# Performance work log

Measured on AMD Instinct MI355X. Metric: run time of the kernel, lower is better.

Reference implementation:

```python
import jax, jax.numpy as jnp
import numpy as np

N = 100000
E = 1600000
D_IN = 128
D_OUT = 128

def setup_inputs() -> dict:
    key = jax.random.key(0)
    k1, k2, k3, k4, k5, k6 = jax.random.split(key, 6)
    h = jax.random.normal(k1, (N, D_IN), dtype=jnp.float32)
    # norm ~ deg^{-1/2}; use positive uniform values as stand-in
    norm = jax.random.uniform(k2, (N, 1), dtype=jnp.float32, minval=0.05, maxval=1.0)
    src = jax.random.randint(k3, (E,), 0, N, dtype=jnp.int32)
    dst = jax.random.randint(k4, (E,), 0, N, dtype=jnp.int32)
    weight = jax.random.normal(k5, (D_IN, D_OUT), dtype=jnp.float32) * (2.0 / (D_IN + D_OUT)) ** 0.5
    bias = jnp.zeros((D_OUT,), dtype=jnp.float32)
    return {"h": h, "norm": norm, "src": src, "dst": dst, "weight": weight, "bias": bias}

def reference(h, norm, src, dst, weight, bias):
    n_nodes = h.shape[0]
    hw = h @ weight                      # [N, D_out] dense GEMM
    hw = hw * norm                       # pre-aggregation degree scale
    msgs = hw[src]                       # gather: [E, D_out]
    agg = jax.ops.segment_sum(msgs, dst, num_segments=n_nodes)  # scatter-sum
    out = agg * norm + bias              # post-scale + bias
    return out
```

## Files before the change

kernel.cpp:

```cpp
#include <hip/hip_runtime.h>
#include <hip/hip_bf16.h>

#define D 128
#define D4 32
#define CHUNK 3072
#define MAXB 2048
#define NSEG 8

typedef __attribute__((ext_vector_type(8))) short bf16x8;
typedef __attribute__((ext_vector_type(4))) float f32x4;

static __device__ __forceinline__ unsigned short f2bf(float f) {
    unsigned u = __float_as_uint(f);
    u += 0x7FFFu + ((u >> 16) & 1u);
    return (unsigned short)(u >> 16);
}
static __device__ __forceinline__ float bf2f(unsigned short u) {
    return __uint_as_float(((unsigned)u) << 16);
}

__global__ __launch_bounds__(256) void gemm_mfma_kernel(
    const float* __restrict__ h, const float* __restrict__ W,
    const float* __restrict__ norm, unsigned short* __restrict__ hwb,
    int n_nodes)
{
    __shared__ unsigned short As[64 * 136];
    __shared__ unsigned short Bs[128 * 136];

    const int t = threadIdx.x;
    const int row0 = blockIdx.x * 64;

    #pragma unroll
    for (int i = 0; i < 16; ++i) {
        const int idx = t + 256 * i;
        const int k = idx >> 5;
        const int c = (idx & 31) * 4;
        const float4 w = ((const float4*)W)[idx];
        Bs[(c + 0) * 136 + k] = f2bf(w.x);
        Bs[(c + 1) * 136 + k] = f2bf(w.y);
        Bs[(c + 2) * 136 + k] = f2bf(w.z);
        Bs[(c + 3) * 136 + k] = f2bf(w.w);
    }
    #pragma unroll
    for (int i = 0; i < 8; ++i) {
        const int idx = t + 256 * i;
        const int r = idx >> 5;
        const int kq = idx & 31;
        long gr = row0 + r; if (gr >= n_nodes) gr = n_nodes - 1;
        const float4 a = ((const float4*)(h + gr * D))[kq];
        ushort4 o;
        o.x = f2bf(a.x); o.y = f2bf(a.y); o.z = f2bf(a.z); o.w = f2bf(a.w);
        *(ushort4*)&As[r * 136 + kq * 4] = o;
    }
    __syncthreads();

    const int wv = t >> 6;
    const int lane = t & 63;
    const int m = lane & 15;
    const int quad = lane >> 4;

    f32x4 acc[8];
    #pragma unroll
    for (int nt = 0; nt < 8; ++nt) { f32x4 z = {0.f, 0.f, 0.f, 0.f}; acc[nt] = z; }

    #pragma unroll
    for (int kt = 0; kt < 4; ++kt) {
        const bf16x8 af = *(const bf16x8*)&As[(wv * 16 + m) * 136 + kt * 32 + quad * 8];
        #pragma unroll
        for (int nt = 0; nt < 8; ++nt) {
            const bf16x8 bfr = *(const bf16x8*)&Bs[(nt * 16 + m) * 136 + kt * 32 + quad * 8];
            acc[nt] = __builtin_amdgcn_mfma_f32_16x16x32_bf16(af, bfr, acc[nt], 0, 0, 0);
        }
    }

    float nv[4];
    #pragma unroll
    for (int i = 0; i < 4; ++i) {
        const int gr = row0 + wv * 16 + quad * 4 + i;
        nv[i] = (gr < n_nodes) ? norm[gr] : 0.f;
    }
    #pragma unroll
    for (int nt = 0; nt < 8; ++nt) {
        #pragma unroll
        for (int i = 0; i < 4; ++i) {
            const int gr = row0 + wv * 16 + quad * 4 + i;
            if (gr < n_nodes)
                hwb[(size_t)gr * D + nt * 16 + m] = f2bf(acc[nt][i] * nv[i]);
        }
    }
}

__global__ __launch_bounds__(1024) void hist_kernel(
    const int* __restrict__ dst, int* __restrict__ H,
    unsigned short* __restrict__ hwb, int n_edges, int n_nodes)
{
    __shared__ int lbh[MAXB];
    const int t = threadIdx.x;
    const int g = blockIdx.x;
    for (int i = t; i < MAXB; i += 1024) lbh[i] = 0;
    if (g == 0 && t < 32) {
        ushort4 z; z.x = z.y = z.z = z.w = 0;
        ((ushort4*)(hwb + (size_t)n_nodes * D))[t] = z;
    }
    __syncthreads();
    const int e0 = g * CHUNK;
    const int e1 = min(e0 + CHUNK, n_edges);
    for (int e = e0 + t; e < e1; e += 1024) {
        atomicAdd(&lbh[dst[e] >> 6], 1);
    }
    __syncthreads();
    for (int i = t; i < MAXB; i += 1024) {
        H[(size_t)g * MAXB + i] = lbh[i];
    }
}

__global__ __launch_bounds__(256) void colsum_kernel(
    const int* __restrict__ H, int* __restrict__ PS, int eb)
{
    const int col = blockIdx.x * 256 + threadIdx.x;
    const int seg = blockIdx.y;
    const int glen = (eb + NSEG - 1) / NSEG;
    const int g0 = seg * glen;
    const int g1 = min(g0 + glen, eb);
    int s = 0;
    for (int g = g0; g < g1; ++g) s += H[(size_t)g * MAXB + col];
    PS[seg * MAXB + col] = s;
}

__global__ __launch_bounds__(256) void bucket_scan_kernel(
    const int* __restrict__ PS, int* __restrict__ boff, int* __restrict__ bcur)
{
    __shared__ int tmp[256];
    const int t = threadIdx.x;
    int v[8];
    int s = 0;
    #pragma unroll
    for (int k = 0; k < 8; ++k) {
        const int i = t * 8 + k;
        int c = 0;
        #pragma unroll
        for (int sg = 0; sg < NSEG; ++sg) c += PS[sg * MAXB + i];
        v[k] = c; s += c;
    }
    tmp[t] = s;
    __syncthreads();
    for (int ofs = 1; ofs < 256; ofs <<= 1) {
        int x = (t >= ofs) ? tmp[t - ofs] : 0;
        __syncthreads();
        tmp[t] += x;
        __syncthreads();
    }
    int run = tmp[t] - s;
    #pragma unroll
    for (int k = 0; k < 8; ++k) {
        boff[t * 8 + k] = run;
        bcur[t * 8 + k] = run;
        run += v[k];
    }
    if (t == 255) boff[MAXB] = run;
}

__global__ __launch_bounds__(1024) void bscatter_kernel(
    const int* __restrict__ src, const int* __restrict__ dst,
    const int* __restrict__ H, int* __restrict__ bcur,
    unsigned int* __restrict__ ebuf, int n_edges)
{
    __shared__ int lbh[MAXB];
    __shared__ int lofs[MAXB];
    const int t = threadIdx.x;
    const int g = blockIdx.x;
    for (int i = t; i < MAXB; i += 1024) {
        lbh[i] = 0;
        const int c = H[(size_t)g * MAXB + i];
        lofs[i] = c ? atomicAdd(&bcur[i], c) : 0;
    }
    __syncthreads();
    const int e0 = g * CHUNK;
    const int e1 = min(e0 + CHUNK, n_edges);
    for (int e = e0 + t; e < e1; e += 1024) {
        const int d = dst[e];
        const int bk = d >> 6;
        const int r = atomicAdd(&lbh[bk], 1);
        ebuf[lofs[bk] + r] = (unsigned)src[e] | ((unsigned)(d & 63) << 17);
    }
}

__global__ __launch_bounds__(256) void fill_local_kernel(
    const unsigned int* __restrict__ ebuf, const int* __restrict__ boff,
    int* __restrict__ off, int* __restrict__ cnt,
    int* __restrict__ srcs, int n_nodes)
{
    __shared__ int lcnt[64];
    __shared__ int lcur[64];
    __shared__ int loff[64];
    const int t = threadIdx.x;
    const int b = blockIdx.x;
    const int gn0 = b * 64;
    if (t < 64) lcnt[t] = 0;
    __syncthreads();
    const int e0 = boff[b], e1 = boff[b + 1];
    for (int e = e0 + t; e < e1; e += 256) {
        atomicAdd(&lcnt[(ebuf[e] >> 17) & 63], 1);
    }
    __syncthreads();
    if (t < 64) {
        const int c = lcnt[t];
        const int p = (c + 7) & ~7;
        int x = p;
        #pragma unroll
        for (int ofs = 1; ofs < 64; ofs <<= 1) {
            const int y = __shfl_up(x, ofs, 64);
            if (t >= ofs) x += y;
        }
        const int base = boff[b] + b * 448 + (x - p);
        lcur[t] = base;
        loff[t] = base;
        const int gn = gn0 + t;
        if (gn < n_nodes) { cnt[gn] = c; off[gn] = base; }
    }
    __syncthreads();
    for (int e = e0 + t; e < e1; e += 256) {
        const unsigned rec = ebuf[e];
        const int loc = (rec >> 17) & 63;
        const int pos = atomicAdd(&lcur[loc], 1);
        srcs[pos] = (int)(rec & 0x1FFFFu);
    }
    for (int w = t; w < 512; w += 256) {
        const int ln = w >> 3, k = w & 7;
        const int gn = gn0 + ln;
        if (gn < n_nodes) {
            const int c = lcnt[ln];
            const int pad = (8 - (c & 7)) & 7;
            if (k < pad) srcs[loff[ln] + c + k] = n_nodes;
        }
    }
}

__global__ __launch_bounds__(256) void agg_kernel(
    const unsigned short* __restrict__ hwb, const int* __restrict__ srcs,
    const int* __restrict__ off, const int* __restrict__ cnt,
    const float* __restrict__ norm, const float* __restrict__ bias,
    float* __restrict__ out, int n_nodes)
{
    const int t = threadIdx.x;
    const int sub = t >> 5;
    const int lane32 = t & 31;
    const int node = blockIdx.x * 8 + sub;
    if (node >= n_nodes) return;

    const int start = off[node];
    const int deg = cnt[node];
    const int nb8 = (deg + 7) >> 3;

    const ushort4* hw4 = (const ushort4*)hwb;

    float4 acc; acc.x = acc.y = acc.z = acc.w = 0.0f;
    int myidx = 0;

    for (int b = 0; b < nb8; ++b) {
        const int q = b & 3;
        if (q == 0) myidx = srcs[start + b * 8 + lane32];
        ushort4 v[8];
        #pragma unroll
        for (int jj = 0; jj < 8; ++jj) {
            const int s = __shfl(myidx, q * 8 + jj, 32);
            v[jj] = hw4[(long)s * D4 + lane32];
        }
        #pragma unroll
        for (int jj = 0; jj < 8; ++jj) {
            acc.x += bf2f(v[jj].x);
            acc.y += bf2f(v[jj].y);
            acc.z += bf2f(v[jj].z);
            acc.w += bf2f(v[jj].w);
        }
    }

    const float nv = norm[node];
    const float4 bs = ((const float4*)bias)[lane32];
    float4 o;
    o.x = acc.x * nv + bs.x;
    o.y = acc.y * nv + bs.y;
    o.z = acc.z * nv + bs.z;
    o.w = acc.w * nv + bs.w;
    ((float4*)out)[(long)node * D4 + lane32] = o;
}

__global__ __launch_bounds__(256) void scatter_kernel(
    const unsigned short* __restrict__ hwb, const int* __restrict__ src,
    const int* __restrict__ dst, float* __restrict__ out, int n_edges)
{
    const int idx = blockIdx.x * 256 + threadIdx.x;
    if (idx >= n_edges * D4) return;
    const int e = idx >> 5;
    const int g = idx & 31;
    const int s = src[e];
    const int d = dst[e];
    const ushort4 v = ((const ushort4*)hwb)[(long)s * D4 + g];
    float* o = out + (long)d * D + g * 4;
    atomicAdd(o + 0, bf2f(v.x));
    atomicAdd(o + 1, bf2f(v.y));
    atomicAdd(o + 2, bf2f(v.z));
    atomicAdd(o + 3, bf2f(v.w));
}

__global__ __launch_bounds__(256) void finalize_kernel(
    float* __restrict__ out, const float* __restrict__ norm,
    const float* __restrict__ bias, int n_nodes)
{
    const int idx = blockIdx.x * 256 + threadIdx.x;
    if (idx >= n_nodes * D4) return;
    const int n = idx >> 5;
    const int g = idx & 31;
    float4 v = ((float4*)out)[idx];
    const float nv = norm[n];
    const float4 b = ((const float4*)bias)[g];
    v.x = v.x * nv + b.x;
    v.y = v.y * nv + b.y;
    v.z = v.z * nv + b.z;
    v.w = v.w * nv + b.w;
    ((float4*)out)[idx] = v;
}

extern "C" void kernel_launch(void* const* d_in, const int* in_sizes, int n_in,
                              void* d_out, int out_size, void* d_ws, size_t ws_size,
                              hipStream_t stream) {
    const float* h    = (const float*)d_in[0];
    const float* norm = (const float*)d_in[1];
    const int*   src  = (const int*)d_in[2];
    const int*   dst  = (const int*)d_in[3];
    const float* W    = (const float*)d_in[4];
    const float* bias = (const float*)d_in[5];
    float* out = (float*)d_out;

    const int n_nodes = in_sizes[1];
    const int n_edges = in_sizes[2];

    const int NBUCK = (n_nodes + 63) >> 6;
    const int EB    = (n_edges + CHUNK - 1) / CHUNK;
    const int srcs_len = n_edges + 448 * NBUCK + 64;

    size_t p = 0;
    auto take = [&](size_t bytes) {
        size_t cur = p;
        p += (bytes + 255) & ~(size_t)255;
        return cur;
    };
    const size_t hwb_off  = take(((size_t)n_nodes + 1) * D * sizeof(unsigned short));
    const size_t cnt_off  = take((size_t)n_nodes * sizeof(int));
    const size_t off_off  = take((size_t)n_nodes * sizeof(int));
    const size_t srcs_off = take((size_t)srcs_len * sizeof(int));
    const size_t ebuf_off = take((size_t)n_edges * sizeof(unsigned int));
    const size_t boff_off = take((MAXB + 1) * sizeof(int));
    const size_t bcur_off = take(MAXB * sizeof(int));
    const size_t H_off    = take((size_t)EB * MAXB * sizeof(int));
    const size_t PS_off   = take((size_t)NSEG * MAXB * sizeof(int));
    const size_t needed = p;

    char* ws = (char*)d_ws;
    unsigned short* hwb = (unsigned short*)(ws + hwb_off);

    gemm_mfma_kernel<<<(n_nodes + 63) / 64, 256, 0, stream>>>(h, W, norm, hwb, n_nodes);

    if (ws_size >= needed && NBUCK <= MAXB && n_nodes <= 131072) {
        int* cnt   = (int*)(ws + cnt_off);
        int* off   = (int*)(ws + off_off);
        int* srcs  = (int*)(ws + srcs_off);
        unsigned int* ebuf = (unsigned int*)(ws + ebuf_off);
        int* boff  = (int*)(ws + boff_off);
        int* bcur  = (int*)(ws + bcur_off);
        int* H     = (int*)(ws + H_off);
        int* PS    = (int*)(ws + PS_off);

        hist_kernel<<<EB, 1024, 0, stream>>>(dst, H, hwb, n_edges, n_nodes);
        colsum_kernel<<<dim3(MAXB / 256, NSEG), 256, 0, stream>>>(H, PS, EB);
        bucket_scan_kernel<<<1, 256, 0, stream>>>(PS, boff, bcur);
        bscatter_kernel<<<EB, 1024, 0, stream>>>(src, dst, H, bcur, ebuf, n_edges);
        fill_local_kernel<<<NBUCK, 256, 0, stream>>>(ebuf, boff, off, cnt, srcs, n_nodes);
        agg_kernel<<<(n_nodes + 7) / 8, 256, 0, stream>>>(hwb, srcs, off, cnt, norm, bias,
                                                          out, n_nodes);
    } else {
        hipMemsetAsync(d_out, 0, (size_t)out_size * sizeof(float), stream);
        const int work = n_edges * D4;
        scatter_kernel<<<(work + 255) / 256, 256, 0, stream>>>(hwb, src, dst, out, n_edges);
        const int work2 = n_nodes * D4;
        finalize_kernel<<<(work2 + 255) / 256, 256, 0, stream>>>(out, norm, bias, n_nodes);
    }
}
```

Baseline: 265.3 us.

## Fuse bucket sort and aggregation into one cooperative persistent kernel

Replaces the chain of six launches (histogram, column sums, scan, scatter, local fill, aggregate) with one cooperative kernel that uses grid-wide syncs between phases. Edge indices are kept in registers between histogram and scatter, and per-bucket source lists are staged in LDS before aggregation. The aim is to remove launch gaps and avoid re-reading src/dst. In exchange each block uses large LDS and 1024 threads, so few blocks fit per CU, and grid.sync has its own cost.

```diff
diff --git a/kernel.cpp b/kernel.cpp
--- a/kernel.cpp
+++ b/kernel.cpp
@@ -1,11 +1,17 @@
 #include <hip/hip_runtime.h>
 #include <hip/hip_bf16.h>
+#include <hip/hip_cooperative_groups.h>
+
+namespace cg = cooperative_groups;
 
 #define D 128
 #define D4 32
 #define CHUNK 3072
+#define CHUNK_C 3200
+#define KSLOT 4
 #define MAXB 2048
 #define NSEG 8
+#define SLDS 8192
 
 typedef __attribute__((ext_vector_type(8))) short bf16x8;
 typedef __attribute__((ext_vector_type(4))) float f32x4;
@@ -86,6 +92,202 @@
             const int gr = row0 + wv * 16 + quad * 4 + i;
             if (gr < n_nodes)
                 hwb[(size_t)gr * D + nt * 16 + m] = f2bf(acc[nt][i] * nv[i]);
+        }
+    }
+}
+
+__global__ __launch_bounds__(1024, 8) void coop_kernel(
+    const int* __restrict__ src, const int* __restrict__ dst,
+    int* __restrict__ H, int* __restrict__ PS, int* __restrict__ SB,
+    int* __restrict__ boff, int* __restrict__ CO,
+    unsigned int* __restrict__ ebuf, int* __restrict__ srcs_g,
+    unsigned short* __restrict__ hwb,
+    const float* __restrict__ norm, const float* __restrict__ bias,
+    float* __restrict__ out,
+    int n_edges, int n_nodes, int EB, int NBUCK)
+{
+    __shared__ int lbh[MAXB];
+    __shared__ int tmp[1024];
+    __shared__ int slds[SLDS];
+    __shared__ int lcnt[64];
+    __shared__ int lcur[64];
+    __shared__ int loffL[64];
+
+    cg::grid_group grid = cg::this_grid();
+    const int t = threadIdx.x;
+    const int g = blockIdx.x;
+    const int gid = g * 1024 + t;
+    const int glen = (EB + NSEG - 1) / NSEG;
+
+    for (int i = t; i < MAXB; i += 1024) lbh[i] = 0;
+    if (g == 0 && t < 32) {
+        ushort4 z; z.x = z.y = z.z = z.w = 0;
+        ((ushort4*)(hwb + (size_t)n_nodes * D))[t] = z;
+    }
+    __syncthreads();
+    const int e0 = g * CHUNK_C;
+    const int e1 = min(e0 + CHUNK_C, n_edges);
+    int ed[KSLOT], es[KSLOT], er[KSLOT];
+    bool ok[KSLOT];
+    #pragma unroll
+    for (int k = 0; k < KSLOT; ++k) {
+        const int e = e0 + t + 1024 * k;
+        ok[k] = e < e1;
+        if (ok[k]) {
+            ed[k] = dst[e];
+            es[k] = src[e];
+            er[k] = atomicAdd(&lbh[ed[k] >> 6], 1);
+        } else { ed[k] = 0; es[k] = 0; er[k] = 0; }
+    }
+    __syncthreads();
+    for (int i = t; i < MAXB; i += 1024) H[(size_t)g * MAXB + i] = lbh[i];
+    grid.sync();
+
+    if (gid < NSEG * MAXB) {
+        const int seg = gid >> 11;
+        const int c = gid & (MAXB - 1);
+        const int g0 = seg * glen, g1 = min(g0 + glen, EB);
+        int s = 0;
+        for (int gg = g0; gg < g1; ++gg) s += H[(size_t)gg * MAXB + c];
+        PS[seg * MAXB + c] = s;
+    }
+    grid.sync();
+
+    if (g == 0) {
+        const int cA = 2 * t, cB = 2 * t + 1;
+        int va = 0, vb = 0;
+        #pragma unroll
+        for (int sg = 0; sg < NSEG; ++sg) { va += PS[sg * MAXB + cA]; vb += PS[sg * MAXB + cB]; }
+        tmp[t] = va + vb;
+        __syncthreads();
+        for (int ofs = 1; ofs < 1024; ofs <<= 1) {
+            const int x = (t >= ofs) ? tmp[t - ofs] : 0;
+            __syncthreads();
+            tmp[t] += x;
+            __syncthreads();
+        }
+        const int run = tmp[t] - (va + vb);
+        boff[cA] = run;
+        boff[cB] = run + va;
+        if (t == 1023) boff[MAXB] = tmp[1023];
+        int sb = run;
+        #pragma unroll
+        for (int sg = 0; sg < NSEG; ++sg) { SB[sg * MAXB + cA] = sb; sb += PS[sg * MAXB + cA]; }
+        sb = run + va;
+        #pragma unroll
+        for (int sg = 0; sg < NSEG; ++sg) { SB[sg * MAXB + cB] = sb; sb += PS[sg * MAXB + cB]; }
+    }
+    grid.sync();
+
+    if (gid < NSEG * MAXB) {
+        const int seg = gid >> 11;
+        const int c = gid & (MAXB - 1);
+        const int g0 = seg * glen, g1 = min(g0 + glen, EB);
+        int run = SB[seg * MAXB + c];
+        for (int gg = g0; gg < g1; ++gg) {
+            CO[(size_t)gg * MAXB + c] = run;
+            run += H[(size_t)gg * MAXB + c];
+        }
+    }
+    grid.sync();
+
+    for (int i = t; i < MAXB; i += 1024) lbh[i] = CO[(size_t)g * MAXB + i];
+    __syncthreads();
+    #pragma unroll
+    for (int k = 0; k < KSLOT; ++k) {
+        if (ok[k])
+            ebuf[lbh[ed[k] >> 6] + er[k]] =
+                (unsigned)es[k] | ((unsigned)(ed[k] & 63) << 17);
+    }
+    grid.sync();
+
+    const ushort4* hw4 = (const ushort4*)hwb;
+    for (int bkt = g; bkt < NBUCK; bkt += gridDim.x) {
+        __syncthreads();
+        if (t < 64) lcnt[t] = 0;
+        __syncthreads();
+        const int w0 = boff[bkt], w1 = boff[bkt + 1];
+        const int wlen = w1 - w0;
+        const bool uselds = (wlen + 480) <= SLDS;
+        const int gbase = w0 + 448 * bkt;
+        for (int e = w0 + t; e < w1; e += 1024)
+            atomicAdd(&lcnt[(ebuf[e] >> 17) & 63], 1);
+        __syncthreads();
+        if (t < 64) {
+            const int c = lcnt[t];
+            const int p = (c + 7) & ~7;
+            int x = p;
+            #pragma unroll
+            for (int ofs = 1; ofs < 64; ofs <<= 1) {
+                const int y = __shfl_up(x, ofs, 64);
+                if (t >= ofs) x += y;
+            }
+            const int base = x - p;
+            lcur[t] = base;
+            loffL[t] = base;
+        }
+        __syncthreads();
+        for (int e = w0 + t; e < w1; e += 1024) {
+            const unsigned rec = ebuf[e];
+            const int loc = (rec >> 17) & 63;
+            const int pos = atomicAdd(&lcur[loc], 1);
+            const int sv = (int)(rec & 0x1FFFFu);
+            if (uselds) slds[pos] = sv; else srcs_g[gbase + pos] = sv;
+        }
+        for (int w = t; w < 512; w += 1024) {
+            const int ln = w >> 3, k = w & 7;
+            const int gn = bkt * 64 + ln;
+            if (gn < n_nodes) {
+                const int c = lcnt[ln];
+                const int pad = (8 - (c & 7)) & 7;
+                if (k < pad) {
+                    const int pos = loffL[ln] + c + k;
+                    if (uselds) slds[pos] = n_nodes; else srcs_g[gbase + pos] = n_nodes;
+                }
+            }
+        }
+        __syncthreads();
+
+        const int grp = t >> 5;
+        const int l = t & 31;
+        #pragma unroll
+        for (int nn = 0; nn < 2; ++nn) {
+            const int loc = grp * 2 + nn;
+            const int gn = bkt * 64 + loc;
+            if (gn >= n_nodes) continue;
+            const int start = loffL[loc];
+            const int deg = lcnt[loc];
+            const int nb8 = (deg + 7) >> 3;
+            float4 acc; acc.x = acc.y = acc.z = acc.w = 0.f;
+            int myidx = 0;
+            for (int b = 0; b < nb8; ++b) {
+                const int q = b & 3;
+                if (q == 0) {
+                    const int ri = start + b * 8 + l;
+                    myidx = uselds ? slds[ri] : srcs_g[gbase + ri];
+                }
+                ushort4 v[8];
+                #pragma unroll
+                for (int jj = 0; jj < 8; ++jj) {
+                    const int s = __shfl(myidx, q * 8 + jj, 32);
+                    v[jj] = hw4[(long)s * D4 + l];
+                }
+                #pragma unroll
+                for (int jj = 0; jj < 8; ++jj) {
+                    acc.x += bf2f(v[jj].x);
+                    acc.y += bf2f(v[jj].y);
+                    acc.z += bf2f(v[jj].z);
+                    acc.w += bf2f(v[jj].w);
+                }
+            }
+            const float nv = norm[gn];
+            const float4 bs = ((const float4*)bias)[l];
+            float4 o;
+            o.x = acc.x * nv + bs.x;
+            o.y = acc.y * nv + bs.y;
+            o.z = acc.z * nv + bs.z;
+            o.w = acc.w * nv + bs.w;
+            ((float4*)out)[(long)gn * D4 + l] = o;
         }
     }
 }
@@ -336,7 +538,9 @@
     const int n_edges = in_sizes[2];
 
     const int NBUCK = (n_nodes + 63) >> 6;
-    const int EB    = (n_edges + CHUNK - 1) / CHUNK;
+    const int EB2   = (n_edges + CHUNK - 1) / CHUNK;
+    const int EBC   = (n_edges + CHUNK_C - 1) / CHUNK_C;
+    const int EBmax = (EB2 > EBC) ? EB2 : EBC;
     const int srcs_len = n_edges + 448 * NBUCK + 64;
 
     size_t p = 0;
@@ -352,8 +556,10 @@
     const size_t ebuf_off = take((size_t)n_edges * sizeof(unsigned int));
     const size_t boff_off = take((MAXB + 1) * sizeof(int));
     const size_t bcur_off = take(MAXB * sizeof(int));
-    const size_t H_off    = take((size_t)EB * MAXB * sizeof(int));
+    const size_t H_off    = take((size_t)EBmax * MAXB * sizeof(int));
     const size_t PS_off   = take((size_t)NSEG * MAXB * sizeof(int));
+    const size_t SB_off   = take((size_t)NSEG * MAXB * sizeof(int));
+    const size_t CO_off   = take((size_t)EBmax * MAXB * sizeof(int));
     const size_t needed = p;
 
     char* ws = (char*)d_ws;
@@ -361,7 +567,46 @@
 
     gemm_mfma_kernel<<<(n_nodes + 63) / 64, 256, 0, stream>>>(h, W, norm, hwb, n_nodes);
 
-    if (ws_size >= needed && NBUCK <= MAXB && n_nodes <= 131072) {
+    static int s_blocks_per_cu = -1;
+    static int s_ncu = 0;
+    if (s_blocks_per_cu < 0) {
+        int nb = 0;
+        if (hipOccupancyMaxActiveBlocksPerMultiprocessor(&nb, coop_kernel, 1024, 0) != hipSuccess)
+            nb = 0;
+        int dev = 0;
+        hipGetDevice(&dev);
+        int ncu = 0;
+        if (hipDeviceGetAttribute(&ncu, hipDeviceAttributeMultiprocessorCount, dev) != hipSuccess)
+            ncu = 0;
+        s_blocks_per_cu = nb;
+        s_ncu = ncu;
+    }
+
+    const bool ws_ok = (ws_size >= needed) && (NBUCK <= MAXB) && (n_nodes <= 131072);
+    const bool coop_ok = ws_ok && EBC >= 16 && EBC <= 512 &&
+                         (long)EBC <= (long)s_blocks_per_cu * (long)s_ncu;
+
+    if (coop_ok) {
+        int* cnt   = (int*)(ws + cnt_off);   (void)cnt;
+        int* off   = (int*)(ws + off_off);   (void)off;
+        int* srcs  = (int*)(ws + srcs_off);
+        unsigned int* ebuf = (unsigned int*)(ws + ebuf_off);
+        int* boff  = (int*)(ws + boff_off);
+        int* H     = (int*)(ws + H_off);
+        int* PS    = (int*)(ws + PS_off);
+        int* SBp   = (int*)(ws + SB_off);
+        int* CO    = (int*)(ws + CO_off);
+
+        int ne = n_edges, nn = n_nodes, eb = EBC, nbk = NBUCK;
+        void* args[] = {
+            (void*)&src, (void*)&dst, (void*)&H, (void*)&PS, (void*)&SBp,
+            (void*)&boff, (void*)&CO, (void*)&ebuf, (void*)&srcs, (void*)&hwb,
+            (void*)&norm, (void*)&bias, (void*)&out,
+            (void*)&ne, (void*)&nn, (void*)&eb, (void*)&nbk
+        };
+        hipLaunchCooperativeKernel((void*)coop_kernel, dim3(EBC), dim3(1024),
+                                   args, 0, stream);
+    } else if (ws_ok && EB2 <= 1024) {
         int* cnt   = (int*)(ws + cnt_off);
         int* off   = (int*)(ws + off_off);
         int* srcs  = (int*)(ws + srcs_off);
@@ -371,10 +616,10 @@
         int* H     = (int*)(ws + H_off);
         int* PS    = (int*)(ws + PS_off);
 
-        hist_kernel<<<EB, 1024, 0, stream>>>(dst, H, hwb, n_edges, n_nodes);
-        colsum_kernel<<<dim3(MAXB / 256, NSEG), 256, 0, stream>>>(H, PS, EB);
+        hist_kernel<<<EB2, 1024, 0, stream>>>(dst, H, hwb, n_edges, n_nodes);
+        colsum_kernel<<<dim3(MAXB / 256, NSEG), 256, 0, stream>>>(H, PS, EB2);
         bucket_scan_kernel<<<1, 256, 0, stream>>>(PS, boff, bcur);
-        bscatter_kernel<<<EB, 1024, 0, stream>>>(src, dst, H, bcur, ebuf, n_edges);
+        bscatter_kernel<<<EB2, 1024, 0, stream>>>(src, dst, H, bcur, ebuf, n_edges);
         fill_local_kernel<<<NBUCK, 256, 0, stream>>>(ebuf, boff, off, cnt, srcs, n_nodes);
         agg_kernel<<<(n_nodes + 7) / 8, 256, 0, stream>>>(hwb, srcs, off, cnt, norm, bias,
                                                           out, n_nodes);
```

After: 263.5 us. No clear change (-0.7%).

## Fuse local CSR fill with aggregation and pre-transpose weight to bf16

Applied to the files above, without the earlier changes.

Merges fill_local and agg kernels so each 64-node bucket builds its source list in LDS and immediately aggregates, removing the global srcs/off/cnt round trip and one launch. The weight fp32-to-bf16 transpose now runs once in a small kernel instead of in every GEMM block, which instead load it with vector copies. In exchange the aggregation runs on only NBUCK (~1563) blocks that each process 64 nodes serially per group, so latency hiding and load balance may be worse. Each block also now uses 16KB more LDS, which can lower occupancy.

```diff
diff --git a/kernel.cpp b/kernel.cpp
--- a/kernel.cpp
+++ b/kernel.cpp
@@ -6,8 +6,10 @@
 #define CHUNK 3072
 #define MAXB 2048
 #define NSEG 8
+#define SL 4096
 
 typedef __attribute__((ext_vector_type(8))) short bf16x8;
+typedef __attribute__((ext_vector_type(8))) unsigned short ushort8;
 typedef __attribute__((ext_vector_type(4))) float f32x4;
 
 static __device__ __forceinline__ unsigned short f2bf(float f) {
@@ -19,8 +21,21 @@
     return __uint_as_float(((unsigned)u) << 16);
 }
 
+__global__ __launch_bounds__(256) void wcvt_kernel(
+    const float* __restrict__ W, unsigned short* __restrict__ Wt)
+{
+    const int idx = blockIdx.x * 256 + threadIdx.x;
+    const float4 w = ((const float4*)W)[idx];
+    const int k = idx >> 5;
+    const int c = (idx & 31) * 4;
+    Wt[(c + 0) * 128 + k] = f2bf(w.x);
+    Wt[(c + 1) * 128 + k] = f2bf(w.y);
+    Wt[(c + 2) * 128 + k] = f2bf(w.z);
+    Wt[(c + 3) * 128 + k] = f2bf(w.w);
+}
+
 __global__ __launch_bounds__(256) void gemm_mfma_kernel(
-    const float* __restrict__ h, const float* __restrict__ W,
+    const float* __restrict__ h, const unsigned short* __restrict__ Wt,
     const float* __restrict__ norm, unsigned short* __restrict__ hwb,
     int n_nodes)
 {
@@ -31,15 +46,12 @@
     const int row0 = blockIdx.x * 64;
 
     #pragma unroll
-    for (int i = 0; i < 16; ++i) {
+    for (int i = 0; i < 8; ++i) {
         const int idx = t + 256 * i;
-        const int k = idx >> 5;
-        const int c = (idx & 31) * 4;
-        const float4 w = ((const float4*)W)[idx];
-        Bs[(c + 0) * 136 + k] = f2bf(w.x);
-        Bs[(c + 1) * 136 + k] = f2bf(w.y);
-        Bs[(c + 2) * 136 + k] = f2bf(w.z);
-        Bs[(c + 3) * 136 + k] = f2bf(w.w);
+        const int c = idx >> 4;
+        const int k8 = idx & 15;
+        const ushort8 w = ((const ushort8*)Wt)[idx];
+        *(ushort8*)&Bs[c * 136 + k8 * 8] = w;
     }
     #pragma unroll
     for (int i = 0; i < 8; ++i) {
@@ -185,21 +197,28 @@
     }
 }
 
-__global__ __launch_bounds__(256) void fill_local_kernel(
+__global__ __launch_bounds__(256) void fillagg_kernel(
     const unsigned int* __restrict__ ebuf, const int* __restrict__ boff,
-    int* __restrict__ off, int* __restrict__ cnt,
-    int* __restrict__ srcs, int n_nodes)
-{
+    int* __restrict__ srcs_g, const unsigned short* __restrict__ hwb,
+    const float* __restrict__ norm, const float* __restrict__ bias,
+    float* __restrict__ out, int n_nodes)
+{
+    __shared__ int slds[SL];
     __shared__ int lcnt[64];
     __shared__ int lcur[64];
     __shared__ int loff[64];
     const int t = threadIdx.x;
     const int b = blockIdx.x;
     const int gn0 = b * 64;
+
     if (t < 64) lcnt[t] = 0;
     __syncthreads();
-    const int e0 = boff[b], e1 = boff[b + 1];
-    for (int e = e0 + t; e < e1; e += 256) {
+    const int w0 = boff[b], w1 = boff[b + 1];
+    const int wlen = w1 - w0;
+    const bool uselds = (wlen + 480) <= SL;
+    const int gbase = w0 + 448 * b;
+
+    for (int e = w0 + t; e < w1; e += 256) {
         atomicAdd(&lcnt[(ebuf[e] >> 17) & 63], 1);
     }
     __syncthreads();
@@ -212,18 +231,17 @@
             const int y = __shfl_up(x, ofs, 64);
             if (t >= ofs) x += y;
         }
-        const int base = boff[b] + b * 448 + (x - p);
+        const int base = x - p;
         lcur[t] = base;
         loff[t] = base;
-        const int gn = gn0 + t;
-        if (gn < n_nodes) { cnt[gn] = c; off[gn] = base; }
-    }
-    __syncthreads();
-    for (int e = e0 + t; e < e1; e += 256) {
+    }
+    __syncthreads();
+    for (int e = w0 + t; e < w1; e += 256) {
         const unsigned rec = ebuf[e];
         const int loc = (rec >> 17) & 63;
         const int pos = atomicAdd(&lcur[loc], 1);
-        srcs[pos] = (int)(rec & 0x1FFFFu);
+        const int sv = (int)(rec & 0x1FFFFu);
+        if (uselds) slds[pos] = sv; else srcs_g[gbase + pos] = sv;
     }
     for (int w = t; w < 512; w += 256) {
         const int ln = w >> 3, k = w & 7;
@@ -231,58 +249,55 @@
         if (gn < n_nodes) {
             const int c = lcnt[ln];
             const int pad = (8 - (c & 7)) & 7;
-            if (k < pad) srcs[loff[ln] + c + k] = n_nodes;
+            if (k < pad) {
+                const int pos = loff[ln] + c + k;
+                if (uselds) slds[pos] = n_nodes; else srcs_g[gbase + pos] = n_nodes;
+            }
         }
     }
-}
-
-__global__ __launch_bounds__(256) void agg_kernel(
-    const unsigned short* __restrict__ hwb, const int* __restrict__ srcs,
-    const int* __restrict__ off, const int* __restrict__ cnt,
-    const float* __restrict__ norm, const float* __restrict__ bias,
-    float* __restrict__ out, int n_nodes)
-{
-    const int t = threadIdx.x;
-    const int sub = t >> 5;
-    const int lane32 = t & 31;
-    const int node = blockIdx.x * 8 + sub;
-    if (node >= n_nodes) return;
-
-    const int start = off[node];
-    const int deg = cnt[node];
-    const int nb8 = (deg + 7) >> 3;
+    __syncthreads();
 
     const ushort4* hw4 = (const ushort4*)hwb;
-
-    float4 acc; acc.x = acc.y = acc.z = acc.w = 0.0f;
-    int myidx = 0;
-
-    for (int b = 0; b < nb8; ++b) {
-        const int q = b & 3;
-        if (q == 0) myidx = srcs[start + b * 8 + lane32];
-        ushort4 v[8];
-        #pragma unroll
-        for (int jj = 0; jj < 8; ++jj) {
-            const int s = __shfl(myidx, q * 8 + jj, 32);
-            v[jj] = hw4[(long)s * D4 + lane32];
+    const int grp = t >> 5;
+    const int l = t & 31;
+    const float4 bs = ((const float4*)bias)[l];
+    for (int nn = 0; nn < 8; ++nn) {
+        const int loc = grp * 8 + nn;
+        const int gn = gn0 + loc;
+        if (gn >= n_nodes) continue;
+        const int start = loff[loc];
+        const int deg = lcnt[loc];
+        const int nb8 = (deg + 7) >> 3;
+        float4 acc; acc.x = acc.y = acc.z = acc.w = 0.f;
+        int myidx = 0;
+        for (int bb = 0; bb < nb8; ++bb) {
+            const int q = bb & 3;
+            if (q == 0) {
+                const int ri = start + bb * 8 + l;
+                myidx = uselds ? slds[ri] : srcs_g[gbase + ri];
+            }
+            ushort4 v[8];
+            #pragma unroll
+            for (int jj = 0; jj < 8; ++jj) {
+                const int s = __shfl(myidx, q * 8 + jj, 32);
+                v[jj] = hw4[(long)s * D4 + l];
+            }
+            #pragma unroll
+            for (int jj = 0; jj < 8; ++jj) {
+                acc.x += bf2f(v[jj].x);
+                acc.y += bf2f(v[jj].y);
+                acc.z += bf2f(v[jj].z);
+                acc.w += bf2f(v[jj].w);
+            }
         }
-        #pragma unroll
-        for (int jj = 0; jj < 8; ++jj) {
-            acc.x += bf2f(v[jj].x);
-            acc.y += bf2f(v[jj].y);
-            acc.z += bf2f(v[jj].z);
-            acc.w += bf2f(v[jj].w);
-        }
-    }
-
-    const float nv = norm[node];
-    const float4 bs = ((const float4*)bias)[lane32];
-    float4 o;
-    o.x = acc.x * nv + bs.x;
-    o.y = acc.y * nv + bs.y;
-    o.z = acc.z * nv + bs.z;
-    o.w = acc.w * nv + bs.w;
-    ((float4*)out)[(long)node * D4 + lane32] = o;
+        const float nv = norm[gn];
+        float4 o;
+        o.x = acc.x * nv + bs.x;
+        o.y = acc.y * nv + bs.y;
+        o.z = acc.z * nv + bs.z;
+        o.w = acc.w * nv + bs.w;
+        ((float4*)out)[(long)gn * D4 + l] = o;
+    }
 }
 
 __global__ __launch_bounds__(256) void scatter_kernel(
@@ -346,8 +361,7 @@
         return cur;
     };
     const size_t hwb_off  = take(((size_t)n_nodes + 1) * D * sizeof(unsigned short));
-    const size_t cnt_off  = take((size_t)n_nodes * sizeof(int));
-    const size_t off_off  = take((size_t)n_nodes * sizeof(int));
+    const size_t wt_off   = take((size_t)D * D * sizeof(unsigned short));
     const size_t srcs_off = take((size_t)srcs_len * sizeof(int));
     const size_t ebuf_off = take((size_t)n_edges * sizeof(unsigned int));
     const size_t boff_off = take((MAXB + 1) * sizeof(int));
@@ -358,12 +372,12 @@
 
     char* ws = (char*)d_ws;
     unsigned short* hwb = (unsigned short*)(ws + hwb_off);
-
-    gemm_mfma_kernel<<<(n_nodes + 63) / 64, 256, 0, stream>>>(h, W, norm, hwb, n_nodes);
-
-    if (ws_size >= needed && NBUCK <= MAXB && n_nodes <= 131072) {
-        int* cnt   = (int*)(ws + cnt_off);
-        int* off   = (int*)(ws + off_off);
+    unsigned short* Wt  = (unsigned short*)(ws + wt_off);
+
+    wcvt_kernel<<<16, 256, 0, stream>>>(W, Wt);
+    gemm_mfma_kernel<<<(n_nodes + 63) / 64, 256, 0, stream>>>(h, Wt, norm, hwb, n_nodes);
+
+    if (ws_size >= needed && NBUCK <= MAXB && n_nodes <= 131072 && EB <= 1024) {
         int* srcs  = (int*)(ws + srcs_off);
         unsigned int* ebuf = (unsigned int*)(ws + ebuf_off);
         int* boff  = (int*)(ws + boff_off);
@@ -375,9 +389,8 @@
         colsum_kernel<<<dim3(MAXB / 256, NSEG), 256, 0, stream>>>(H, PS, EB);
         bucket_scan_kernel<<<1, 256, 0, stream>>>(PS, boff, bcur);
         bscatter_kernel<<<EB, 1024, 0, stream>>>(src, dst, H, bcur, ebuf, n_edges);
-        fill_local_kernel<<<NBUCK, 256, 0, stream>>>(ebuf, boff, off, cnt, srcs, n_nodes);
-        agg_kernel<<<(n_nodes + 7) / 8, 256, 0, stream>>>(hwb, srcs, off, cnt, norm, bias,
-                                                          out, n_nodes);
+        fillagg_kernel<<<NBUCK, 256, 0, stream>>>(ebuf, boff, srcs, hwb, norm, bias,
+                                                  out, n_nodes);
     } else {
         hipMemsetAsync(d_out, 0, (size_t)out_size * sizeof(float), stream);
         const int work = n_edges * D4;
```

New measurement: 250.8 us. 1.06x faster.
